# Optimization experiments

Measured on AMD Instinct MI355X. Metric: run time of the kernel, lower is better.

The kernel has to match this reference:

```python
import jax, jax.numpy as jnp
import numpy as np
import math

N_HEADS = 16
DIM_MODEL = 1024
DIM_KQ = 64
DIM_V = 64
B, T = 2, 2048


def setup_inputs() -> dict:
    key = jax.random.key(0)
    ks = jax.random.split(key, 9)
    s = 1.0 / math.sqrt(DIM_MODEL)
    return {
        "x": jax.random.normal(ks[0], (B, T, DIM_MODEL), dtype=jnp.float32),
        "Wq": jax.random.normal(ks[1], (DIM_MODEL, N_HEADS * DIM_KQ), dtype=jnp.float32) * s,
        "bq": jnp.zeros((N_HEADS * DIM_KQ,), dtype=jnp.float32),
        "Wk": jax.random.normal(ks[2], (DIM_MODEL, N_HEADS * DIM_KQ), dtype=jnp.float32) * s,
        "bk": jnp.zeros((N_HEADS * DIM_KQ,), dtype=jnp.float32),
        "Wv": jax.random.normal(ks[3], (DIM_MODEL, N_HEADS * DIM_V), dtype=jnp.float32) * s,
        "bv": jnp.zeros((N_HEADS * DIM_V,), dtype=jnp.float32),
        "Wo": jax.random.normal(ks[4], (N_HEADS * DIM_V, DIM_MODEL), dtype=jnp.float32) * s,
        "bo": jnp.zeros((DIM_MODEL,), dtype=jnp.float32),
    }


def reference(x, Wq, bq, Wk, bk, Wv, bv, Wo, bo):
    b, t, _ = x.shape
    # projections, split into heads: [B, T, h, d]
    q = (x @ Wq + bq).reshape(b, t, N_HEADS, DIM_KQ)
    k = (x @ Wk + bk).reshape(b, t, N_HEADS, DIM_KQ)
    v = (x @ Wv + bv).reshape(b, t, N_HEADS, DIM_V)
    # NOTE: faithful to source einsum 'B Tq h d, B Tk h d -> B h Tk Tq'
    # scores[b, h, tk, tq] = q[b, tq] . k[b, tk]
    scores = jnp.einsum('bqhd,bkhd->bhkq', q, k)
    # softmax over the LAST axis (= query axis tq), as in the source
    attn = jax.nn.softmax(scores / math.sqrt(DIM_KQ), axis=-1)
    # source einsum 'B h Tk Tq, B Tq h dv -> B Tq h dv':
    # sums over Tk only -> out[b, tq, h, dv] = v[b, tq, h, dv] * sum_tk attn[b, h, tk, tq]
    colsum = attn.sum(axis=2)                      # [B, h, Tq]
    mixed = v * colsum.transpose(0, 2, 1)[..., None]  # [B, Tq, h, dv]
    out = mixed.reshape(b, t, N_HEADS * DIM_V) @ Wo + bo
    return out
```

## Files before the change

kernel.cpp:

```cpp
#include <hip/hip_runtime.h>
#include <hip/hip_bf16.h>
#include <stdint.h>

typedef __attribute__((ext_vector_type(4))) float f32x4;
typedef __attribute__((ext_vector_type(8))) __bf16 bf16x8;

#define AS1 __attribute__((address_space(1)))
#define AS3 __attribute__((address_space(3)))

#if __has_builtin(__builtin_amdgcn_exp2f)
#define EXP2(x) __builtin_amdgcn_exp2f(x)
#else
#define EXP2(x) exp2f(x)
#endif

__device__ __forceinline__ ushort f2bf(float f) {
  uint32_t u = __builtin_bit_cast(uint32_t, f);
  u += 0x7fffu + ((u >> 16) & 1u);
  return (ushort)(u >> 16);
}
__device__ __forceinline__ float bf2f(ushort h) {
  uint32_t u = ((uint32_t)h) << 16;
  return __builtin_bit_cast(float, u);
}

#define SCK 0.18033688011112042f

#define GLD(src, dst) \
  __builtin_amdgcn_global_load_lds((const AS1 uint32_t*)(src), (AS3 uint32_t*)(dst), 16, 0, 0)

#define BARRIER()                          \
  do {                                     \
    __builtin_amdgcn_sched_barrier(0);     \
    __builtin_amdgcn_s_barrier();          \
    __builtin_amdgcn_sched_barrier(0);     \
  } while (0)


__global__ void k_cvt_x(const float* __restrict__ x, ushort* __restrict__ xb, int n4) {
  int i = blockIdx.x * blockDim.x + threadIdx.x;
  if (i >= n4) return;
  float4 v = ((const float4*)x)[i];
  ushort4 o;
  o.x = f2bf(v.x); o.y = f2bf(v.y); o.z = f2bf(v.z); o.w = f2bf(v.w);
  ((ushort4*)xb)[i] = o;
}

__global__ void k_prep_w(const float* __restrict__ Wq, const float* __restrict__ Wk,
                         const float* __restrict__ Wv, const float* __restrict__ Wo,
                         ushort* __restrict__ Wt, ushort* __restrict__ Wot) {
  __shared__ float tile[32][33];
  int z = blockIdx.z;
  const float* src = (z == 0) ? Wq : (z == 1) ? Wk : (z == 2) ? Wv : Wo;
  ushort* dst = (z < 3) ? (Wt + (size_t)z * 1048576) : Wot;
  float scale = (z == 1) ? SCK : 1.0f;
  int k0 = blockIdx.y * 32, n0 = blockIdx.x * 32;
  int tx = threadIdx.x, ty = threadIdx.y;
#pragma unroll
  for (int i = 0; i < 4; i++)
    tile[ty + i * 8][tx] = src[(size_t)(k0 + ty + i * 8) * 1024 + n0 + tx];
  __syncthreads();
#pragma unroll
  for (int i = 0; i < 4; i++)
    dst[(size_t)(n0 + ty + i * 8) * 1024 + k0 + tx] = f2bf(tile[tx][ty + i * 8] * scale);
}

template <int MODE>
__global__ __launch_bounds__(512, 2) void k_gemm8(const ushort* __restrict__ A,
                                                  const ushort* __restrict__ Bt,
                                                  void* __restrict__ Cv,
                                                  const float* __restrict__ b0,
                                                  const float* __restrict__ b1,
                                                  const float* __restrict__ b2,
                                                  int K, int ldc) {
  __shared__ char ldsb[131072];
  const int tid = threadIdx.x;
  const int lane = tid & 63;
  const int wid = tid >> 6;
  const int wr = wid >> 2, wc = wid & 3;
  const int l15 = lane & 15, l4 = lane >> 4;
  const int row0 = blockIdx.y * 256;
  const int col0 = blockIdx.x * 256;
  const int T = K >> 5;

  const int swz = ((tid & 3) ^ ((tid >> 3) & 3)) << 3;
  const ushort* Ap = A + (size_t)(row0 + (tid >> 2)) * K + swz;
  const ushort* Bp = Bt + (size_t)(col0 + (tid >> 2)) * K + swz;

#define STAGE_H1(t)                              \
  do {                                           \
    char* bufs = ldsb + (((t) & 3) << 15);       \
    const ushort* pa = Ap + (size_t)(t) * 32;    \
    GLD(pa, bufs + tid * 16);                    \
    GLD(pa + 128 * K, bufs + 8192 + tid * 16);   \
  } while (0)
#define STAGE_H2(t)                              \
  do {                                           \
    char* bufs = ldsb + (((t) & 3) << 15);       \
    const ushort* pb = Bp + (size_t)(t) * 32;    \
    GLD(pb, bufs + 16384 + tid * 16);            \
    GLD(pb + 128 * K, bufs + 24576 + tid * 16);  \
  } while (0)

  int aoffL[8], boffL[4];
#pragma unroll
  for (int m = 0; m < 8; m++) {
    int r = wr * 128 + m * 16 + l15;
    aoffL[m] = r * 64 + ((l4 ^ ((r >> 1) & 3)) << 4);
  }
#pragma unroll
  for (int n = 0; n < 4; n++) {
    int r = wc * 64 + n * 16 + l15;
    boffL[n] = 16384 + r * 64 + ((l4 ^ ((r >> 1) & 3)) << 4);
  }

  f32x4 acc[8][4] = {};

  STAGE_H1(0); STAGE_H2(0);
  STAGE_H1(1); STAGE_H2(1);
  STAGE_H1(2); STAGE_H2(2);
  asm volatile("s_waitcnt vmcnt(8)" ::: "memory");
  BARRIER();

#define PHASE(t, DO_STAGE, VMSTR)                                                     \
  do {                                                                                \
    char* buf = ldsb + (((t) & 3) << 15);                                             \
    {                                                                                 \
      bf16x8 af[4], bfr[4];                                                           \
      _Pragma("unroll") for (int m = 0; m < 4; m++)                                   \
          af[m] = *(const bf16x8*)(buf + aoffL[m]);                                   \
      _Pragma("unroll") for (int n = 0; n < 4; n++)                                   \
          bfr[n] = *(const bf16x8*)(buf + boffL[n]);                                  \
      if (DO_STAGE) STAGE_H1((t) + 3);                                                \
      BARRIER();                                                                      \
      __builtin_amdgcn_s_setprio(1);                                                  \
      _Pragma("unroll") for (int m = 0; m < 4; m++)                                   \
          _Pragma("unroll") for (int n = 0; n < 4; n++)                               \
              acc[m][n] = __builtin_amdgcn_mfma_f32_16x16x32_bf16(af[m], bfr[n],      \
                                                                  acc[m][n], 0, 0, 0);\
      __builtin_amdgcn_s_setprio(0);                                                  \
      BARRIER();                                                                      \
      bf16x8 af2[4];                                                                  \
      _Pragma("unroll") for (int m = 0; m < 4; m++)                                   \
          af2[m] = *(const bf16x8*)(buf + aoffL[m + 4]);                              \
      if (DO_STAGE) STAGE_H2((t) + 3);                                                \
      BARRIER();                                                                      \
      __builtin_amdgcn_s_setprio(1);                                                  \
      _Pragma("unroll") for (int m = 0; m < 4; m++)                                   \
          _Pragma("unroll") for (int n = 0; n < 4; n++)                               \
              acc[m + 4][n] = __builtin_amdgcn_mfma_f32_16x16x32_bf16(                \
                  af2[m], bfr[n], acc[m + 4][n], 0, 0, 0);                            \
      __builtin_amdgcn_s_setprio(0);                                                  \
      asm volatile(VMSTR ::: "memory");                                               \
      BARRIER();                                                                      \
    }                                                                                 \
  } while (0)

  for (int t = 0; t < T - 3; ++t) PHASE(t, true, "s_waitcnt vmcnt(8)");
  PHASE(T - 3, false, "s_waitcnt vmcnt(4)");
  PHASE(T - 2, false, "s_waitcnt vmcnt(0)");
  PHASE(T - 1, false, "s_nop 0");

#undef PHASE
#undef STAGE_H1
#undef STAGE_H2

#pragma unroll
  for (int m = 0; m < 8; m++)
#pragma unroll
    for (int n = 0; n < 4; n++) {
      int colg = col0 + wc * 64 + n * 16 + l15;
      float bias;
      if (MODE == 0) {
        bias = (colg < 1024) ? b0[colg]
                             : ((colg < 2048) ? b1[colg - 1024] * SCK : b2[colg - 2048]);
      } else {
        bias = b0[colg];
      }
#pragma unroll
      for (int j = 0; j < 4; j++) {
        int rowg = row0 + wr * 128 + m * 16 + l4 * 4 + j;
        float v = acc[m][n][j] + bias;
        if (MODE == 0)
          ((ushort*)Cv)[(size_t)rowg * ldc + colg] = f2bf(v);
        else
          ((float*)Cv)[(size_t)rowg * ldc + colg] = v;
      }
    }
}

template <int MODE>
__global__ __launch_bounds__(256) void k_gemm(const ushort* __restrict__ A,
                                              const ushort* __restrict__ Bt,
                                              void* __restrict__ Cv,
                                              const float* __restrict__ b0,
                                              int M, int N, int K, int ldc) {
  __shared__ ushort As[128 * 32];
  __shared__ ushort Bs[128 * 32];
  const int tid = threadIdx.x;
  const int lane = tid & 63;
  const int wid = tid >> 6;
  const int wr = wid >> 1, wc = wid & 1;
  const int row0 = blockIdx.y * 128;
  const int col0 = blockIdx.x * 128;
  const int l15 = lane & 15, l4 = lane >> 4;

  f32x4 acc[4][4] = {};

  for (int k0 = 0; k0 < K; k0 += 32) {
    __syncthreads();
#pragma unroll
    for (int i = 0; i < 2; i++) {
      int c = i * 256 + tid;
      int r = c >> 2, cb = c & 3;
      GLD(A + (size_t)(row0 + r) * K + k0 + cb * 8, (char*)As + c * 16);
      GLD(Bt + (size_t)(col0 + r) * K + k0 + cb * 8, (char*)Bs + c * 16);
    }
    __syncthreads();
    bf16x8 av[4], bv[4];
#pragma unroll
    for (int m = 0; m < 4; m++)
      av[m] = *(const bf16x8*)(As + (wr * 64 + m * 16 + l15) * 32 + l4 * 8);
#pragma unroll
    for (int n = 0; n < 4; n++)
      bv[n] = *(const bf16x8*)(Bs + (wc * 64 + n * 16 + l15) * 32 + l4 * 8);
#pragma unroll
    for (int m = 0; m < 4; m++)
#pragma unroll
      for (int n = 0; n < 4; n++)
        acc[m][n] = __builtin_amdgcn_mfma_f32_16x16x32_bf16(av[m], bv[n], acc[m][n], 0, 0, 0);
  }

#pragma unroll
  for (int m = 0; m < 4; m++)
#pragma unroll
    for (int n = 0; n < 4; n++) {
      int colg = col0 + wc * 64 + n * 16 + l15;
      float bias = b0[colg];
#pragma unroll
      for (int j = 0; j < 4; j++) {
        int rowg = row0 + wr * 64 + m * 16 + l4 * 4 + j;
        float v = acc[m][n][j] + bias;
        if (MODE == 0)
          ((ushort*)Cv)[(size_t)rowg * ldc + colg] = f2bf(v);
        else
          ((float*)Cv)[(size_t)rowg * ldc + colg] = v;
      }
    }
}

__global__ __launch_bounds__(256, 2) void k_attn_z(const ushort* __restrict__ QKV,
                                                   float* __restrict__ Zpart) {
  const int bid = blockIdx.x;
  const int xcd = bid & 7, kk = bid >> 3;
  const int g = xcd * 8 + (kk >> 3);
  const int tkb = kk & 7;
  const int bh = g & 31, s = g >> 5;
  const int b = bh >> 4, h = bh & 15;
  const int tid = threadIdx.x, lane = tid & 63, w = tid >> 6;
  const int l15 = lane & 15, l4 = lane >> 4;
  const size_t rs = 3072;

  __shared__ ushort Ks[256 * 64];
  __shared__ ushort Qs[2][128 * 64];

  const ushort* Kbase = QKV + (size_t)(b * 2048 + tkb * 256) * rs + 1024 + h * 64;
  const ushort* Qbase = QKV + (size_t)(b * 2048 + s * 1024) * rs + h * 64;

  const int csl = ((tid & 7) ^ ((tid >> 3) & 7)) * 8;

#pragma unroll
  for (int i = 0; i < 8; i++) {
    int c = i * 256 + tid;
    GLD(Kbase + (size_t)(c >> 3) * rs + csl, (char*)Ks + c * 16);
  }
  const ushort* gq[4];
#pragma unroll
  for (int i = 0; i < 4; i++) {
    int c = i * 256 + tid;
    gq[i] = Qbase + (size_t)(c >> 3) * rs + csl;
    GLD(gq[i], (char*)Qs[0] + c * 16);
  }
  asm volatile("s_waitcnt vmcnt(0)" ::: "memory");
  BARRIER();

  bf16x8 kf[4][2];
#pragma unroll
  for (int m = 0; m < 4; m++)
#pragma unroll
    for (int d = 0; d < 2; d++) {
      int r = w * 64 + m * 16 + l15;
      kf[m][d] = *(const bf16x8*)((const char*)Ks + r * 128 + (((d * 4 + l4) ^ (r & 7)) << 4));
    }

  float z[4][4] = {};
  const f32x4 zero4 = {0.f, 0.f, 0.f, 0.f};

  for (int t = 0; t < 8; ++t) {
    if (t < 7) {
      char* qd = (char*)Qs[(t + 1) & 1];
#pragma unroll
      for (int i = 0; i < 4; i++) {
        int c = i * 256 + tid;
        GLD(gq[i] + (size_t)(t + 1) * 128 * rs, qd + c * 16);
      }
    }
    const char* qb = (const char*)Qs[t & 1];
    f32x4 acc[4][8];
    __builtin_amdgcn_s_setprio(1);
#pragma unroll
    for (int d = 0; d < 2; d++)
#pragma unroll
      for (int n = 0; n < 8; n++) {
        int r = n * 16 + l15;
        bf16x8 qf = *(const bf16x8*)(qb + r * 128 + (((d * 4 + l4) ^ (r & 7)) << 4));
#pragma unroll
        for (int m = 0; m < 4; m++)
          acc[m][n] = __builtin_amdgcn_mfma_f32_16x16x32_bf16(
              kf[m][d], qf, d == 0 ? zero4 : acc[m][n], 0, 0, 0);
      }
    __builtin_amdgcn_s_setprio(0);
#pragma unroll
    for (int m = 0; m < 4; m++)
#pragma unroll
      for (int n = 0; n < 8; n++)
#pragma unroll
        for (int j = 0; j < 4; j++) z[m][j] += EXP2(acc[m][n][j]);
    if (t < 7) {
      asm volatile("s_waitcnt vmcnt(0)" ::: "memory");
      BARRIER();
    }
  }

#pragma unroll
  for (int m = 0; m < 4; m++)
#pragma unroll
    for (int j = 0; j < 4; j++) {
      float v = z[m][j];
      v += __shfl_xor(v, 1, 64);
      v += __shfl_xor(v, 2, 64);
      v += __shfl_xor(v, 4, 64);
      v += __shfl_xor(v, 8, 64);
      if (l15 == 0)
        Zpart[(size_t)s * 65536 + bh * 2048 + tkb * 256 + w * 64 + m * 16 + l4 * 4 + j] = v;
    }
}

__global__ void k_rz(const float* __restrict__ Zpart, float* __restrict__ rrz) {
  int g = blockIdx.x * 256 + threadIdx.x;
  rrz[g] = 1.0f / (Zpart[g] + Zpart[65536 + g]);
}

__global__ __launch_bounds__(256, 2) void k_attn_cs(const ushort* __restrict__ QKV,
                                                    const float* __restrict__ rrz,
                                                    float* __restrict__ csPart) {
  const int bid = blockIdx.x;
  const int xcd = bid & 7, kk = bid >> 3;
  const int g = xcd * 8 + (kk >> 3);
  const int tqb = kk & 7;
  const int bh = g & 31, s = g >> 5;
  const int b = bh >> 4, h = bh & 15;
  const int tid = threadIdx.x, lane = tid & 63, w = tid >> 6;
  const int l15 = lane & 15, l4 = lane >> 4;
  const size_t rs = 3072;

  __shared__ ushort Qs[256 * 64];
  __shared__ ushort Ks[2][128 * 64];

  const ushort* Qbase = QKV + (size_t)(b * 2048 + tqb * 256) * rs + h * 64;
  const ushort* Kbase = QKV + (size_t)(b * 2048 + s * 1024) * rs + 1024 + h * 64;
  const float* rz0 = rrz + bh * 2048 + s * 1024;

  const int csl = ((tid & 7) ^ ((tid >> 3) & 7)) * 8;

#pragma unroll
  for (int i = 0; i < 8; i++) {
    int c = i * 256 + tid;
    GLD(Qbase + (size_t)(c >> 3) * rs + csl, (char*)Qs + c * 16);
  }
  const ushort* gk[4];
#pragma unroll
  for (int i = 0; i < 4; i++) {
    int c = i * 256 + tid;
    gk[i] = Kbase + (size_t)(c >> 3) * rs + csl;
    GLD(gk[i], (char*)Ks[0] + c * 16);
  }
  asm volatile("s_waitcnt vmcnt(0)" ::: "memory");
  BARRIER();

  bf16x8 qf[4][2];
#pragma unroll
  for (int m = 0; m < 4; m++)
#pragma unroll
    for (int d = 0; d < 2; d++) {
      int r = w * 64 + m * 16 + l15;
      qf[m][d] = *(const bf16x8*)((const char*)Qs + r * 128 + (((d * 4 + l4) ^ (r & 7)) << 4));
    }

  float cs[4][4] = {};
  const f32x4 zero4 = {0.f, 0.f, 0.f, 0.f};

  for (int t = 0; t < 8; ++t) {
    if (t < 7) {
      char* kd = (char*)Ks[(t + 1) & 1];
#pragma unroll
      for (int i = 0; i < 4; i++) {
        int c = i * 256 + tid;
        GLD(gk[i] + (size_t)(t + 1) * 128 * rs, kd + c * 16);
      }
    }
    float rz[8];
#pragma unroll
    for (int n = 0; n < 8; n++) rz[n] = rz0[t * 128 + n * 16 + l15];
    const char* kb = (const char*)Ks[t & 1];
    f32x4 acc[4][8];
    __builtin_amdgcn_s_setprio(1);
#pragma unroll
    for (int d = 0; d < 2; d++)
#pragma unroll
      for (int n = 0; n < 8; n++) {
        int r = n * 16 + l15;
        bf16x8 kft = *(const bf16x8*)(kb + r * 128 + (((d * 4 + l4) ^ (r & 7)) << 4));
#pragma unroll
        for (int m = 0; m < 4; m++)
          acc[m][n] = __builtin_amdgcn_mfma_f32_16x16x32_bf16(
              qf[m][d], kft, d == 0 ? zero4 : acc[m][n], 0, 0, 0);
      }
    __builtin_amdgcn_s_setprio(0);
#pragma unroll
    for (int m = 0; m < 4; m++)
#pragma unroll
      for (int n = 0; n < 8; n++)
#pragma unroll
        for (int j = 0; j < 4; j++)
          cs[m][j] = fmaf(EXP2(acc[m][n][j]), rz[n], cs[m][j]);
    if (t < 7) {
      asm volatile("s_waitcnt vmcnt(0)" ::: "memory");
      BARRIER();
    }
  }

#pragma unroll
  for (int m = 0; m < 4; m++)
#pragma unroll
    for (int j = 0; j < 4; j++) {
      float v = cs[m][j];
      v += __shfl_xor(v, 1, 64);
      v += __shfl_xor(v, 2, 64);
      v += __shfl_xor(v, 4, 64);
      v += __shfl_xor(v, 8, 64);
      if (l15 == 0)
        csPart[(size_t)s * 65536 + bh * 2048 + tqb * 256 + w * 64 + m * 16 + l4 * 4 + j] = v;
    }
}

__global__ void k_mixed(const ushort* __restrict__ QKV, const float* __restrict__ csPart,
                        ushort* __restrict__ mixed) {
  int i = blockIdx.x * 256 + threadIdx.x;
  int row = i >> 7;
  int col = (i & 127) * 8;
  int b = row >> 11, t = row & 2047, h = col >> 6;
  int g = ((b << 4) + h) * 2048 + t;
  float cs = csPart[g] + csPart[65536 + g];
  uint4 raw = *(const uint4*)(QKV + (size_t)row * 3072 + 2048 + col);
  const ushort* pv = (const ushort*)&raw;
  ushort o[8];
#pragma unroll
  for (int k = 0; k < 8; k++) o[k] = f2bf(bf2f(pv[k]) * cs);
  *(uint4*)(mixed + (size_t)row * 1024 + col) = *(uint4*)o;
}


extern "C" void kernel_launch(void* const* d_in, const int* in_sizes, int n_in,
                              void* d_out, int out_size, void* d_ws, size_t ws_size,
                              hipStream_t stream) {
  const float* x = (const float*)d_in[0];
  const float* Wq = (const float*)d_in[1];
  const float* bq = (const float*)d_in[2];
  const float* Wk = (const float*)d_in[3];
  const float* bk = (const float*)d_in[4];
  const float* Wv = (const float*)d_in[5];
  const float* bv = (const float*)d_in[6];
  const float* Wo = (const float*)d_in[7];
  const float* bo = (const float*)d_in[8];

  char* ws = (char*)d_ws;
  ushort* xb     = (ushort*)(ws);
  ushort* Wt     = (ushort*)(ws + 8388608);
  ushort* Wot    = (ushort*)(ws + 14680064);
  ushort* QKV    = (ushort*)(ws + 16777216);
  float* Zpart   = (float*)(ws + 41943040);
  float* rrz     = (float*)(ws + 42467328);
  float* csPart  = (float*)(ws + 42729472);
  ushort* mixed  = (ushort*)(ws + 43253760);

  k_cvt_x<<<4096, 256, 0, stream>>>(x, xb, 4096 * 1024 / 4);
  k_prep_w<<<dim3(32, 32, 4), dim3(32, 8), 0, stream>>>(Wq, Wk, Wv, Wo, Wt, Wot);

  k_gemm8<0><<<dim3(12, 16), 512, 0, stream>>>(xb, Wt, QKV, bq, bk, bv, 1024, 3072);
  k_attn_z<<<512, 256, 0, stream>>>(QKV, Zpart);
  k_rz<<<256, 256, 0, stream>>>(Zpart, rrz);
  k_attn_cs<<<512, 256, 0, stream>>>(QKV, rrz, csPart);
  k_mixed<<<2048, 256, 0, stream>>>(QKV, csPart, mixed);
  k_gemm<1><<<dim3(8, 32), 256, 0, stream>>>(mixed, Wot, d_out, bo, 4096, 1024, 1024, 1024);
}
```

Before: 135.5 us.

## Restructure QKV GEMM to K=64 double-buffered stages with XCD-aware tile remap

The QKV projection GEMM now stages 64-wide K slices in two 64KB LDS buffers instead of four 32-wide buffers. It uses an 8-way XOR swizzle and splits each iteration into four MFMA quadrants, with loads for stage t+2 interleaved between them. Both GEMMs switch to a 1D grid whose block index is remapped so consecutive tiles land on the same XCD, which is meant to improve L2 reuse. The goal is fewer barriers per unit of K and better overlap of global loads with MFMA work. The cost is more register pressure from the fragment arrays and a shallower prefetch depth.

```diff
diff --git a/kernel.cpp b/kernel.cpp
--- a/kernel.cpp
+++ b/kernel.cpp
@@ -72,98 +72,145 @@
                                                   const float* __restrict__ b0,
                                                   const float* __restrict__ b1,
                                                   const float* __restrict__ b2,
-                                                  int K, int ldc) {
+                                                  int K, int N, int ldc) {
   __shared__ char ldsb[131072];
   const int tid = threadIdx.x;
   const int lane = tid & 63;
   const int wid = tid >> 6;
   const int wr = wid >> 2, wc = wid & 3;
   const int l15 = lane & 15, l4 = lane >> 4;
-  const int row0 = blockIdx.y * 256;
-  const int col0 = blockIdx.x * 256;
-  const int T = K >> 5;
-
-  const int swz = ((tid & 3) ^ ((tid >> 3) & 3)) << 3;
-  const ushort* Ap = A + (size_t)(row0 + (tid >> 2)) * K + swz;
-  const ushort* Bp = Bt + (size_t)(col0 + (tid >> 2)) * K + swz;
-
-#define STAGE_H1(t)                              \
-  do {                                           \
-    char* bufs = ldsb + (((t) & 3) << 15);       \
-    const ushort* pa = Ap + (size_t)(t) * 32;    \
-    GLD(pa, bufs + tid * 16);                    \
-    GLD(pa + 128 * K, bufs + 8192 + tid * 16);   \
+
+  const int L = blockIdx.x;
+  const int f = (L & 7) * ((int)gridDim.x >> 3) + (L >> 3);
+  const int nbx = N >> 8;
+  const int row0 = (f / nbx) * 256;
+  const int col0 = (f % nbx) * 256;
+  const int T = K >> 6;
+
+  const int r3 = tid >> 3, sl = tid & 7;
+  const int cswz = (sl ^ (r3 & 7)) * 8;
+  const ushort* Ap = A + (size_t)(row0 + r3) * K + cswz;
+  const ushort* Bp = Bt + (size_t)(col0 + r3) * K + cswz;
+
+#define STAGE_A8(tt)                                          \
+  do {                                                        \
+    char* dst = ldsb + (((tt) & 1) << 16) + tid * 16;         \
+    const ushort* src = Ap + (size_t)(tt) * 64;               \
+    GLD(src, dst);                                            \
+    GLD(src + 64 * (size_t)K, dst + 8192);                    \
+    GLD(src + 128 * (size_t)K, dst + 16384);                  \
+    GLD(src + 192 * (size_t)K, dst + 24576);                  \
   } while (0)
-#define STAGE_H2(t)                              \
-  do {                                           \
-    char* bufs = ldsb + (((t) & 3) << 15);       \
-    const ushort* pb = Bp + (size_t)(t) * 32;    \
-    GLD(pb, bufs + 16384 + tid * 16);            \
-    GLD(pb + 128 * K, bufs + 24576 + tid * 16);  \
+#define STAGE_B8(tt)                                          \
+  do {                                                        \
+    char* dst = ldsb + (((tt) & 1) << 16) + 32768 + tid * 16; \
+    const ushort* src = Bp + (size_t)(tt) * 64;               \
+    GLD(src, dst);                                            \
+    GLD(src + 64 * (size_t)K, dst + 8192);                    \
+    GLD(src + 128 * (size_t)K, dst + 16384);                  \
+    GLD(src + 192 * (size_t)K, dst + 24576);                  \
   } while (0)
 
-  int aoffL[8], boffL[4];
-#pragma unroll
-  for (int m = 0; m < 8; m++) {
-    int r = wr * 128 + m * 16 + l15;
-    aoffL[m] = r * 64 + ((l4 ^ ((r >> 1) & 3)) << 4);
-  }
-#pragma unroll
-  for (int n = 0; n < 4; n++) {
-    int r = wc * 64 + n * 16 + l15;
-    boffL[n] = 16384 + r * 64 + ((l4 ^ ((r >> 1) & 3)) << 4);
-  }
+  int sfrag[2];
+  sfrag[0] = l15 * 128 + ((l4 ^ (l15 & 7)) << 4);
+  sfrag[1] = l15 * 128 + (((4 + l4) ^ (l15 & 7)) << 4);
 
   f32x4 acc[8][4] = {};
 
-  STAGE_H1(0); STAGE_H2(0);
-  STAGE_H1(1); STAGE_H2(1);
-  STAGE_H1(2); STAGE_H2(2);
+  STAGE_B8(0); STAGE_A8(0);
+  STAGE_B8(1); STAGE_A8(1);
   asm volatile("s_waitcnt vmcnt(8)" ::: "memory");
+  __builtin_amdgcn_sched_barrier(0);
   BARRIER();
 
-#define PHASE(t, DO_STAGE, VMSTR)                                                     \
-  do {                                                                                \
-    char* buf = ldsb + (((t) & 3) << 15);                                             \
-    {                                                                                 \
-      bf16x8 af[4], bfr[4];                                                           \
-      _Pragma("unroll") for (int m = 0; m < 4; m++)                                   \
-          af[m] = *(const bf16x8*)(buf + aoffL[m]);                                   \
-      _Pragma("unroll") for (int n = 0; n < 4; n++)                                   \
-          bfr[n] = *(const bf16x8*)(buf + boffL[n]);                                  \
-      if (DO_STAGE) STAGE_H1((t) + 3);                                                \
-      BARRIER();                                                                      \
-      __builtin_amdgcn_s_setprio(1);                                                  \
-      _Pragma("unroll") for (int m = 0; m < 4; m++)                                   \
-          _Pragma("unroll") for (int n = 0; n < 4; n++)                               \
-              acc[m][n] = __builtin_amdgcn_mfma_f32_16x16x32_bf16(af[m], bfr[n],      \
-                                                                  acc[m][n], 0, 0, 0);\
-      __builtin_amdgcn_s_setprio(0);                                                  \
-      BARRIER();                                                                      \
-      bf16x8 af2[4];                                                                  \
-      _Pragma("unroll") for (int m = 0; m < 4; m++)                                   \
-          af2[m] = *(const bf16x8*)(buf + aoffL[m + 4]);                              \
-      if (DO_STAGE) STAGE_H2((t) + 3);                                                \
-      BARRIER();                                                                      \
-      __builtin_amdgcn_s_setprio(1);                                                  \
-      _Pragma("unroll") for (int m = 0; m < 4; m++)                                   \
-          _Pragma("unroll") for (int n = 0; n < 4; n++)                               \
-              acc[m + 4][n] = __builtin_amdgcn_mfma_f32_16x16x32_bf16(                \
-                  af2[m], bfr[n], acc[m + 4][n], 0, 0, 0);                            \
-      __builtin_amdgcn_s_setprio(0);                                                  \
-      asm volatile(VMSTR ::: "memory");                                               \
-      BARRIER();                                                                      \
-    }                                                                                 \
-  } while (0)
-
-  for (int t = 0; t < T - 3; ++t) PHASE(t, true, "s_waitcnt vmcnt(8)");
-  PHASE(T - 3, false, "s_waitcnt vmcnt(4)");
-  PHASE(T - 2, false, "s_waitcnt vmcnt(0)");
-  PHASE(T - 1, false, "s_nop 0");
-
-#undef PHASE
-#undef STAGE_H1
-#undef STAGE_H2
+  for (int t = 0; t < T; ++t) {
+    char* bb = ldsb + ((t & 1) << 16);
+    const char* Ab = bb + wr * 16384;
+    const char* Bb = bb + 32768 + (wc >> 1) * 16384 + (wc & 1) * 8192;
+    bf16x8 a0[4][2], a1[4][2], b0f[2][2], b1f[2][2];
+
+#pragma unroll
+    for (int m = 0; m < 4; m++)
+#pragma unroll
+      for (int ks = 0; ks < 2; ks++)
+        a0[m][ks] = *(const bf16x8*)(Ab + m * 2048 + sfrag[ks]);
+#pragma unroll
+    for (int n = 0; n < 2; n++)
+#pragma unroll
+      for (int ks = 0; ks < 2; ks++)
+        b0f[n][ks] = *(const bf16x8*)(Bb + n * 2048 + sfrag[ks]);
+    BARRIER();
+    __builtin_amdgcn_s_setprio(1);
+#pragma unroll
+    for (int m = 0; m < 4; m++)
+#pragma unroll
+      for (int n = 0; n < 2; n++)
+#pragma unroll
+        for (int ks = 0; ks < 2; ks++)
+          acc[m][n] = __builtin_amdgcn_mfma_f32_16x16x32_bf16(a0[m][ks], b0f[n][ks],
+                                                              acc[m][n], 0, 0, 0);
+    __builtin_amdgcn_s_setprio(0);
+    BARRIER();
+
+#pragma unroll
+    for (int n = 0; n < 2; n++)
+#pragma unroll
+      for (int ks = 0; ks < 2; ks++)
+        b1f[n][ks] = *(const bf16x8*)(Bb + (n + 2) * 2048 + sfrag[ks]);
+    BARRIER();
+    __builtin_amdgcn_s_setprio(1);
+#pragma unroll
+    for (int m = 0; m < 4; m++)
+#pragma unroll
+      for (int n = 0; n < 2; n++)
+#pragma unroll
+        for (int ks = 0; ks < 2; ks++)
+          acc[m][n + 2] = __builtin_amdgcn_mfma_f32_16x16x32_bf16(a0[m][ks], b1f[n][ks],
+                                                                  acc[m][n + 2], 0, 0, 0);
+    __builtin_amdgcn_s_setprio(0);
+    BARRIER();
+
+#pragma unroll
+    for (int m = 0; m < 4; m++)
+#pragma unroll
+      for (int ks = 0; ks < 2; ks++)
+        a1[m][ks] = *(const bf16x8*)(Ab + 8192 + m * 2048 + sfrag[ks]);
+    if (t < T - 2) STAGE_B8(t + 2);
+    BARRIER();
+    __builtin_amdgcn_s_setprio(1);
+#pragma unroll
+    for (int m = 0; m < 4; m++)
+#pragma unroll
+      for (int n = 0; n < 2; n++)
+#pragma unroll
+        for (int ks = 0; ks < 2; ks++)
+          acc[m + 4][n + 2] = __builtin_amdgcn_mfma_f32_16x16x32_bf16(
+              a1[m][ks], b1f[n][ks], acc[m + 4][n + 2], 0, 0, 0);
+    __builtin_amdgcn_s_setprio(0);
+    BARRIER();
+
+    if (t < T - 2) STAGE_A8(t + 2);
+    BARRIER();
+    __builtin_amdgcn_s_setprio(1);
+#pragma unroll
+    for (int m = 0; m < 4; m++)
+#pragma unroll
+      for (int n = 0; n < 2; n++)
+#pragma unroll
+        for (int ks = 0; ks < 2; ks++)
+          acc[m + 4][n] = __builtin_amdgcn_mfma_f32_16x16x32_bf16(a1[m][ks], b0f[n][ks],
+                                                                  acc[m + 4][n], 0, 0, 0);
+    __builtin_amdgcn_s_setprio(0);
+    if (t < T - 2)
+      asm volatile("s_waitcnt vmcnt(8)" ::: "memory");
+    else if (t == T - 2)
+      asm volatile("s_waitcnt vmcnt(0)" ::: "memory");
+    __builtin_amdgcn_sched_barrier(0);
+    BARRIER();
+  }
+
+#undef STAGE_A8
+#undef STAGE_B8
 
 #pragma unroll
   for (int m = 0; m < 8; m++)
@@ -201,8 +248,11 @@
   const int lane = tid & 63;
   const int wid = tid >> 6;
   const int wr = wid >> 1, wc = wid & 1;
-  const int row0 = blockIdx.y * 128;
-  const int col0 = blockIdx.x * 128;
+  const int L = blockIdx.x;
+  const int f = (L & 7) * ((int)gridDim.x >> 3) + (L >> 3);
+  const int nbx = N >> 7;
+  const int row0 = (f / nbx) * 128;
+  const int col0 = (f % nbx) * 128;
   const int l15 = lane & 15, l4 = lane >> 4;
 
   f32x4 acc[4][4] = {};
@@ -497,10 +547,10 @@
   k_cvt_x<<<4096, 256, 0, stream>>>(x, xb, 4096 * 1024 / 4);
   k_prep_w<<<dim3(32, 32, 4), dim3(32, 8), 0, stream>>>(Wq, Wk, Wv, Wo, Wt, Wot);
 
-  k_gemm8<0><<<dim3(12, 16), 512, 0, stream>>>(xb, Wt, QKV, bq, bk, bv, 1024, 3072);
+  k_gemm8<0><<<192, 512, 0, stream>>>(xb, Wt, QKV, bq, bk, bv, 1024, 3072, 3072);
   k_attn_z<<<512, 256, 0, stream>>>(QKV, Zpart);
   k_rz<<<256, 256, 0, stream>>>(Zpart, rrz);
   k_attn_cs<<<512, 256, 0, stream>>>(QKV, rrz, csPart);
   k_mixed<<<2048, 256, 0, stream>>>(QKV, csPart, mixed);
-  k_gemm<1><<<dim3(8, 32), 256, 0, stream>>>(mixed, Wot, d_out, bo, 4096, 1024, 1024, 1024);
-}
+  k_gemm<1><<<256, 256, 0, stream>>>(mixed, Wot, d_out, bo, 4096, 1024, 1024, 1024);
+}
```

After: 137.3 us. No clear change (+1.4%).
